# Optimization experiments

Hardware: AMD Instinct MI355X
Metric: run time of the kernel (lower is better)

Reference implementation:

```python
import jax, jax.numpy as jnp
import numpy as np

N_IN, N_OUT, D_IN, D_HID, STYLE = 16384, 16384, 64, 256, 64
E = 1048576
EPS_BN = 1e-5
EPS_ADA = 1e-8
SLOPE = 0.2

def leaky(x):
    return jnp.where(x >= 0, x, SLOPE * x)

def bn_train(h, g, b):
    # BatchNorm1d, training mode: batch stats over dim 0, biased variance
    m = jnp.mean(h, axis=0)
    v = jnp.var(h, axis=0)
    return (h - m) * jax.lax.rsqrt(v + EPS_BN) * g + b

def adain(h, style, w1, b1, w2, b2):
    # per-node instance norm over feature axis (unbiased std, as torch.std),
    # style-conditioned per-feature gamma/beta
    mean = jnp.mean(h, axis=1, keepdims=True)
    std = jnp.std(h, axis=1, ddof=1, keepdims=True)
    gamma = w1 @ style + b1
    beta = w2 @ style + b2
    return gamma * (h - mean) / (std + EPS_ADA) + beta

def gat_conv(h, src, dst, W, att_src, att_dst, bias):
    # PyG GATConv, heads=1: linear -> edge attention -> segment softmax -> scatter
    xs = h @ W.T                          # [N, D_IN]
    a_s = xs @ att_src                    # [N]
    a_d = xs @ att_dst                    # [N]
    e = leaky(a_s[src] + a_d[dst])        # [E]
    emax = jax.ops.segment_max(e, dst, num_segments=N_OUT)
    emax = jnp.where(jnp.isfinite(emax), emax, 0.0)
    ex = jnp.exp(e - emax[dst])
    den = jax.ops.segment_sum(ex, dst, num_segments=N_OUT)
    alpha = ex / den[dst]                 # softmax over incoming edges per dst
    out = jax.ops.segment_sum(alpha[:, None] * xs[src], dst, num_segments=N_OUT)
    return out + bias

def setup_inputs():
    key = jax.random.key(0)
    ks = jax.random.split(key, 24)
    p = lambda k, shape: jax.random.normal(k, shape, jnp.float32) * 0.05
    return {
        "x": jax.random.normal(ks[0], (N_IN, D_IN), jnp.float32),
        "style": jax.random.normal(ks[1], (STYLE,), jnp.float32),
        "edge_index": jax.random.randint(ks[2], (2, E), 0, N_OUT, jnp.int32),
        "trs_w": p(ks[3], (N_OUT, N_IN)), "trs_b": jnp.zeros((N_OUT,), jnp.float32),
        "bn2_g": jnp.ones((N_OUT,), jnp.float32), "bn2_b": jnp.zeros((N_OUT,), jnp.float32),
        "fc1_w": p(ks[4], (D_HID, D_IN)), "fc1_b": jnp.zeros((D_HID,), jnp.float32),
        "bn1_g": jnp.ones((D_HID,), jnp.float32), "bn1_b": jnp.zeros((D_HID,), jnp.float32),
        "gat_w": p(ks[5], (D_IN, D_HID)),
        "gat_att_src": p(ks[6], (D_IN,)), "gat_att_dst": p(ks[7], (D_IN,)),
        "gat_b": jnp.zeros((D_IN,), jnp.float32),
        "a1_w1": p(ks[8], (D_IN, STYLE)), "a1_b1": jnp.zeros((D_IN,), jnp.float32),
        "a1_w2": p(ks[9], (D_IN, STYLE)), "a1_b2": jnp.zeros((D_IN,), jnp.float32),
        "a2_w1": p(ks[10], (D_HID, STYLE)), "a2_b1": jnp.zeros((D_HID,), jnp.float32),
        "a2_w2": p(ks[11], (D_HID, STYLE)), "a2_b2": jnp.zeros((D_HID,), jnp.float32),
        "a3_w1": p(ks[12], (D_IN, STYLE)), "a3_b1": jnp.zeros((D_IN,), jnp.float32),
        "a3_w2": p(ks[13], (D_IN, STYLE)), "a3_b2": jnp.zeros((D_IN,), jnp.float32),
    }

def reference(x, style, edge_index, trs_w, trs_b, bn2_g, bn2_b, fc1_w, fc1_b, bn1_g, bn1_b, gat_w, gat_att_src, gat_att_dst, gat_b, a1_w1, a1_b1, a1_w2, a1_b2, a2_w1, a2_b1, a2_w2, a2_b2, a3_w1, a3_b1, a3_w2, a3_b2):
    h = x.T @ trs_w.T + trs_b                 # [D_IN, N_OUT]
    h = leaky(bn_train(h, bn2_g, bn2_b))      # dropout: eval-mode identity
    h = h.T                                    # [N_OUT, D_IN]
    h = adain(h, style, a1_w1, a1_b1, a1_w2, a1_b2)
    h = leaky(bn_train(h @ fc1_w.T + fc1_b, bn1_g, bn1_b))  # [N_OUT, D_HID]
    h = adain(h, style, a2_w1, a2_b1, a2_w2, a2_b2)
    src, dst = edge_index[0], edge_index[1]
    h = leaky(gat_conv(h, src, dst, gat_w, gat_att_src, gat_att_dst, gat_b))
    h = adain(h, style, a3_w1, a3_b1, a3_w2, a3_b2)
    return h
```

## Files before the change

### kernel.cpp

```cpp
#include <hip/hip_runtime.h>
#include <hip/hip_bf16.h>

#define N_NODES 16384
#define NEDGE   1048576

typedef __attribute__((ext_vector_type(4))) float f32x4;
typedef __attribute__((ext_vector_type(4))) unsigned u32x4;
typedef __attribute__((ext_vector_type(8))) short bf16x8;
typedef unsigned short u16;

__device__ __forceinline__ short f2bf(float f) {
  union { float f; unsigned u; } v; v.f = f;
  unsigned r = v.u + 0x7FFFu + ((v.u >> 16) & 1u);
  return (short)(r >> 16);
}
__device__ __forceinline__ unsigned pk2(float lo, float hi) {
  __hip_bfloat162 h = __float22bfloat162_rn(make_float2(lo, hi));
  return *reinterpret_cast<unsigned*>(&h);
}
__device__ __forceinline__ bf16x8 cvt8(f32x4 a, f32x4 b) {
  u32x4 u;
  u[0] = pk2(a[0], a[1]); u[1] = pk2(a[2], a[3]);
  u[2] = pk2(b[0], b[1]); u[3] = pk2(b[2], b[3]);
  return __builtin_bit_cast(bf16x8, u);
}
__device__ __forceinline__ float red16(float v) {
  v += __shfl_xor(v, 1); v += __shfl_xor(v, 2);
  v += __shfl_xor(v, 4); v += __shfl_xor(v, 8);
  return v;
}
__device__ __forceinline__ float red64(float v) {
  v += __shfl_xor(v, 1); v += __shfl_xor(v, 2); v += __shfl_xor(v, 4);
  v += __shfl_xor(v, 8); v += __shfl_xor(v, 16); v += __shfl_xor(v, 32);
  return v;
}
__device__ __forceinline__ float lrelu(float x){ return x >= 0.f ? x : 0.2f*x; }

__global__ __launch_bounds__(256) void k_prep(
    const float* __restrict__ x, const float* __restrict__ style,
    const float* __restrict__ fc1_w, const float* __restrict__ gat_w,
    const float* __restrict__ a1w1, const float* __restrict__ a1b1,
    const float* __restrict__ a1w2, const float* __restrict__ a1b2,
    const float* __restrict__ a2w1, const float* __restrict__ a2b1,
    const float* __restrict__ a2w2, const float* __restrict__ a2b2,
    const float* __restrict__ a3w1, const float* __restrict__ a3b1,
    const float* __restrict__ a3w2, const float* __restrict__ a3b2,
    u16* __restrict__ xpk, u16* __restrict__ fc1pk, u16* __restrict__ gatpk,
    float* __restrict__ gb, const int* __restrict__ dst, int* __restrict__ cnt)
{
  if (blockIdx.x >= 531) {
    int t = ((blockIdx.x - 531) << 8) + threadIdx.x;
    #pragma unroll
    for (int i = 0; i < 4; ++i) atomicAdd(&cnt[dst[t + i*262144]], 1);
    return;
  }
  int tid = blockIdx.x * 256 + threadIdx.x;
  if (tid < 131072) {
    int lane = tid & 63;
    int kt = tid >> 8, nt = (tid >> 6) & 3;
    int k0 = kt*32 + (lane>>4)*8, c = nt*16 + (lane&15);
    bf16x8 o;
    #pragma unroll
    for (int j = 0; j < 8; ++j) o[j] = f2bf(x[(size_t)(k0+j)*64 + c]);
    ((bf16x8*)xpk)[tid] = o;
  } else if (tid < 133120) {
    int t2 = tid - 131072;
    int lane = t2 & 63, kt = t2 >> 10, nt = (t2 >> 6) & 15;
    int k0 = kt*32 + (lane>>4)*8, c = nt*16 + (lane&15);
    bf16x8 o;
    #pragma unroll
    for (int j = 0; j < 8; ++j) o[j] = f2bf(fc1_w[(size_t)c*64 + k0 + j]);
    ((bf16x8*)fc1pk)[t2] = o;
  } else if (tid < 135168) {
    int t3 = tid - 133120;
    int lane = t3 & 63, kt = t3 >> 8, nt = (t3 >> 6) & 3;
    int k0 = kt*32 + (lane>>4)*8, c = nt*16 + (lane&15);
    bf16x8 o;
    #pragma unroll
    for (int j = 0; j < 8; ++j) o[j] = f2bf(gat_w[(size_t)c*256 + k0 + j]);
    ((bf16x8*)gatpk)[t3] = o;
  } else if (tid < 135936) {
    int t4 = tid - 135168;
    const float* wp; const float* bp; float* op; int d;
    if (t4 < 64)       { wp=a1w1; bp=a1b1; op=gb;       d=t4; }
    else if (t4 < 128) { wp=a1w2; bp=a1b2; op=gb+64;    d=t4-64; }
    else if (t4 < 384) { wp=a2w1; bp=a2b1; op=gb+128;   d=t4-128; }
    else if (t4 < 640) { wp=a2w2; bp=a2b2; op=gb+384;   d=t4-384; }
    else if (t4 < 704) { wp=a3w1; bp=a3b1; op=gb+640;   d=t4-640; }
    else               { wp=a3w2; bp=a3b2; op=gb+704;   d=t4-704; }
    float s = bp[d];
    for (int k = 0; k < 64; ++k) s += wp[(size_t)d*64 + k] * style[k];
    op[d] = s;
  }
}

__global__ __launch_bounds__(256, 4) void k_gemm12(
    const float* __restrict__ W, const u16* __restrict__ xpk,
    const float* __restrict__ trs_b, const float* __restrict__ bn2_g,
    const float* __restrict__ bn2_b, const float* __restrict__ g1,
    const float* __restrict__ be1,
    const u16* __restrict__ fc1pk, const float* __restrict__ fc1_b,
    float* __restrict__ H3, float* __restrict__ colsum, float* __restrict__ colsq)
{
  const int tid  = threadIdx.x;
  const int lane = tid & 63;
  const int wv   = tid >> 6;
  const int jb   = blockIdx.x << 4;
  const int c0   = lane & 15, kg = lane >> 4;
  const int sw   = c0 & 7;

  __shared__ __align__(16) float lbuf[2][4096];
  __shared__ float h2t[16 * 68];

  const float* gsrc[4];
  int ldst[4];
  #pragma unroll
  for (int i = 0; i < 4; ++i) {
    int r = wv + (i << 2);
    gsrc[i] = W + (size_t)(jb + r) * 16384 + (size_t)((lane ^ (r & 7)) << 2);
    ldst[i] = ((r << 6) + lane) << 2;
  }

  const int it0 = blockIdx.x & 63;
  f32x4 z = {0.f,0.f,0.f,0.f};
  f32x4 acc = z;

  {
    int kk = it0 << 8;
    #pragma unroll
    for (int i = 0; i < 4; ++i) {
      f32x4 v = __builtin_nontemporal_load((const f32x4*)(gsrc[i] + kk));
      *(f32x4*)&lbuf[0][ldst[i]] = v;
    }
  }
  __syncthreads();

  const bf16x8* xb = ((const bf16x8*)xpk) + (wv << 6) + lane;

  int buf = 0;
  for (int it = 0; it < 64; ++it) {
    f32x4 vn[4];
    const bool hasNext = (it + 1) < 64;
    if (hasNext) {
      int kk = ((it + 1 + it0) & 63) << 8;
      #pragma unroll
      for (int i = 0; i < 4; ++i)
        vn[i] = __builtin_nontemporal_load((const f32x4*)(gsrc[i] + kk));
    }
    {
      int ktg0 = ((it + it0) & 63) << 3;
      const float* lb = lbuf[buf] + (c0 << 8);
      const bf16x8* bp = xb + (size_t)ktg0 * 256;
      #pragma unroll
      for (int kt = 0; kt < 8; ++kt) {
        int u0 = (kt << 3) + (kg << 1);
        f32x4 a0 = *(const f32x4*)(lb + ((u0 ^ sw) << 2));
        f32x4 a1 = *(const f32x4*)(lb + (((u0 + 1) ^ sw) << 2));
        bf16x8 b = bp[(size_t)kt << 8];
        acc = __builtin_amdgcn_mfma_f32_16x16x32_bf16(cvt8(a0, a1), b, acc, 0,0,0);
      }
    }
    if (hasNext) {
      float* lo = lbuf[buf ^ 1];
      #pragma unroll
      for (int i = 0; i < 4; ++i) *(f32x4*)&lo[ldst[i]] = vn[i];
    }
    __syncthreads();
    buf ^= 1;
  }

  #pragma unroll
  for (int i = 0; i < 4; ++i)
    h2t[((kg << 2) + i) * 68 + (wv << 4) + c0] = acc[i];
  __syncthreads();

  #pragma unroll
  for (int i = 0; i < 4; ++i) {
    int jr = (wv << 2) + i;
    int j  = jb + jr;
    float v = h2t[jr * 68 + lane] + trs_b[j];
    float s = red64(v), q = red64(v * v);
    float mean = s * 0.015625f;
    float var  = q * 0.015625f - mean * mean;
    float inv  = rsqrtf(var + 1e-5f) * bn2_g[j];
    v = lrelu((v - mean) * inv + bn2_b[j]);
    s = red64(v); q = red64(v * v);
    mean = s * 0.015625f;
    var  = q * 0.015625f - mean * mean;
    float sd = sqrtf(fmaxf(var, 0.f) * (64.f / 63.f));
    float id = 1.f / (sd + 1e-8f);
    h2t[jr * 68 + lane] = g1[lane] * (v - mean) * id + be1[lane];
  }
  __syncthreads();

  const float* ha = h2t + c0 * 68 + (kg << 3);
  bf16x8 a0 = cvt8(*(const f32x4*)ha,        *(const f32x4*)(ha+4));
  bf16x8 a1 = cvt8(*(const f32x4*)(ha+32),   *(const f32x4*)(ha+36));
  const bf16x8* fpv = ((const bf16x8*)fc1pk) + lane;
  f32x4 acc2[4] = {z,z,z,z};
  #pragma unroll
  for (int q = 0; q < 4; ++q) {
    int nt = (wv << 2) | q;
    acc2[q] = __builtin_amdgcn_mfma_f32_16x16x32_bf16(a0, fpv[nt*64],      acc2[q], 0,0,0);
    acc2[q] = __builtin_amdgcn_mfma_f32_16x16x32_bf16(a1, fpv[(16+nt)*64], acc2[q], 0,0,0);
  }
  #pragma unroll
  for (int q = 0; q < 4; ++q) {
    int c = (((wv << 2) | q) << 4) + c0;
    float bias = fc1_b[c];
    float cs = 0.f, cq = 0.f;
    #pragma unroll
    for (int r = 0; r < 4; ++r) {
      float v = acc2[q][r] + bias;
      H3[(size_t)(jb + (kg<<2) + r) * 256 + c] = v;
      cs += v; cq += v*v;
    }
    cs += __shfl_xor(cs, 16); cs += __shfl_xor(cs, 32);
    cq += __shfl_xor(cq, 16); cq += __shfl_xor(cq, 32);
    if (kg == 0) { atomicAdd(&colsum[c], cs); atomicAdd(&colsq[c], cq); }
  }
}

__global__ __launch_bounds__(256) void k_gemm3(
    const float* __restrict__ H3, const float* __restrict__ colsum,
    const float* __restrict__ colsq, const float* __restrict__ bn1_g,
    const float* __restrict__ bn1_b, const float* __restrict__ gb,
    const u16* __restrict__ gatpk,
    const float* __restrict__ att_s, const float* __restrict__ att_d,
    float* __restrict__ xs, float* __restrict__ a_s, float* __restrict__ a_d,
    const int* __restrict__ cnt, int* __restrict__ off, int* __restrict__ cur)
{
  if (blockIdx.x == 1024) {
    __shared__ int ps[256];
    int t = threadIdx.x;
    int base = t * 64;
    int s = 0;
    for (int i = 0; i < 64; ++i) s += cnt[base + i];
    ps[t] = s;
    __syncthreads();
    for (int d = 1; d < 256; d <<= 1) {
      int v = (t >= d) ? ps[t - d] : 0;
      __syncthreads();
      ps[t] += v;
      __syncthreads();
    }
    int run = ps[t] - s;
    for (int i = 0; i < 64; ++i) {
      off[base + i] = run; cur[base + i] = run;
      run += cnt[base + i];
    }
    return;
  }
  const int lane = threadIdx.x & 63, wv = threadIdx.x >> 6;
  const int jb = blockIdx.x << 4;
  const int c0 = lane & 15, kg = lane >> 4;
  const int row = jb + c0;
  const int col0 = (wv << 6) + (kg << 3);
  const float* g2  = gb + 128;
  const float* be2 = gb + 384;

  f32x4 w4[4];
  float ps = 0.f, pq = 0.f;
  #pragma unroll
  for (int kk = 0; kk < 2; ++kk) {
    #pragma unroll
    for (int h = 0; h < 2; ++h) {
      int c = col0 + kk*32 + h*4;
      f32x4 v  = *(const f32x4*)(H3 + (size_t)row*256 + c);
      f32x4 cm = *(const f32x4*)(colsum + c);
      f32x4 cq = *(const f32x4*)(colsq + c);
      f32x4 gg = *(const f32x4*)(bn1_g + c);
      f32x4 bb = *(const f32x4*)(bn1_b + c);
      f32x4 t;
      #pragma unroll
      for (int i = 0; i < 4; ++i) {
        float m  = cm[i] * (1.f/16384.f);
        float va = cq[i] * (1.f/16384.f) - m*m;
        float u  = (v[i]-m) * rsqrtf(va + 1e-5f) * gg[i] + bb[i];
        u = lrelu(u);
        t[i] = u; ps += u; pq += u*u;
      }
      w4[kk*2+h] = t;
    }
  }
  ps += __shfl_xor(ps, 16); ps += __shfl_xor(ps, 32);
  pq += __shfl_xor(pq, 16); pq += __shfl_xor(pq, 32);
  __shared__ float sps[64], sqs[64];
  if (kg == 0) { sps[(wv<<4) + c0] = ps; sqs[(wv<<4) + c0] = pq; }
  __syncthreads();
  float rs = sps[c0] + sps[16+c0] + sps[32+c0] + sps[48+c0];
  float rq = sqs[c0] + sqs[16+c0] + sqs[32+c0] + sqs[48+c0];
  float mean = rs * (1.f/256.f);
  float var  = rq * (1.f/256.f) - mean*mean;
  float sd   = sqrtf(fmaxf(var, 0.f) * (256.f/255.f));
  float id   = 1.f / (sd + 1e-8f);
  bf16x8 afr[2];
  #pragma unroll
  for (int kk = 0; kk < 2; ++kk) {
    f32x4 o[2];
    #pragma unroll
    for (int h = 0; h < 2; ++h) {
      int c = col0 + kk*32 + h*4;
      f32x4 ga = *(const f32x4*)(g2 + c);
      f32x4 bd = *(const f32x4*)(be2 + c);
      #pragma unroll
      for (int i = 0; i < 4; ++i) o[h][i] = ga[i]*(w4[kk*2+h][i]-mean)*id + bd[i];
    }
    afr[kk] = cvt8(o[0], o[1]);
  }
  const bf16x8* bpv = ((const bf16x8*)gatpk) + lane;
  f32x4 z = {0.f,0.f,0.f,0.f};
  f32x4 acc[4] = {z,z,z,z};
  #pragma unroll
  for (int kk = 0; kk < 2; ++kk) {
    int kt = (wv << 1) | kk;
    #pragma unroll
    for (int nt = 0; nt < 4; ++nt)
      acc[nt] = __builtin_amdgcn_mfma_f32_16x16x32_bf16(afr[kk], bpv[((kt<<2)+nt)*64], acc[nt], 0,0,0);
  }
  __shared__ float lred[3 * 16 * 64];
  if (wv) {
    float* rp = lred + ((wv - 1) << 10) + lane;
    #pragma unroll
    for (int nt = 0; nt < 4; ++nt)
      #pragma unroll
      for (int r = 0; r < 4; ++r) rp[((nt<<2)+r)<<6] = acc[nt][r];
  }
  __syncthreads();
  if (wv) return;
  float as0 = att_s[c0], as1 = att_s[c0+16], as2 = att_s[c0+32], as3 = att_s[c0+48];
  float ad0 = att_d[c0], ad1 = att_d[c0+16], ad2 = att_d[c0+32], ad3 = att_d[c0+48];
  const float* rp = lred + lane;
  #pragma unroll
  for (int r = 0; r < 4; ++r) {
    int j = jb + (kg << 2) + r;
    float v[4];
    #pragma unroll
    for (int nt = 0; nt < 4; ++nt) {
      int idx = ((nt<<2)+r)<<6;
      v[nt] = acc[nt][r] + rp[idx] + rp[idx+1024] + rp[idx+2048];
    }
    float* op = xs + (size_t)j * 64 + c0;
    op[0] = v[0]; op[16] = v[1]; op[32] = v[2]; op[48] = v[3];
    float ss = red16(v[0]*as0 + v[1]*as1 + v[2]*as2 + v[3]*as3);
    float dd = red16(v[0]*ad0 + v[1]*ad1 + v[2]*ad2 + v[3]*ad3);
    if (c0 == 0) { a_s[j] = ss; a_d[j] = dd; }
  }
}

__global__ __launch_bounds__(256) void k_scatter(
    const int* __restrict__ src, const int* __restrict__ dst,
    int* __restrict__ cur, int* __restrict__ ssrc)
{
  int t = (blockIdx.x << 8) + threadIdx.x;
  #pragma unroll
  for (int i = 0; i < 4; ++i) {
    int e = t + i * 262144;
    int s = src[e], d = dst[e];
    int p = atomicAdd(&cur[d], 1);
    ssrc[p] = s;
  }
}

__global__ __launch_bounds__(256) void k_gat(
    const int* __restrict__ cnt, const int* __restrict__ off,
    const int* __restrict__ ssrc, const float* __restrict__ a_s,
    const float* __restrict__ a_d,
    const float* __restrict__ xs, const float* __restrict__ gat_b,
    const float* __restrict__ g3, const float* __restrict__ be3,
    float* __restrict__ out)
{
  const int lane = threadIdx.x & 63, wv = threadIdx.x >> 6;
  const int j = (blockIdx.x << 2) | wv;
  const int n = cnt[j], beg = off[j];
  const int c4 = (lane & 15) << 2;
  const int eq = lane >> 4;
  const float adj = a_d[j];
  f32x4 acc = {0.f,0.f,0.f,0.f};
  float den = 0.f;
  if (n > 0) {
    for (int ch = 0; ch < n; ch += 64) {
      int k = ch + lane;
      bool ok = k < n;
      int   s = ok ? ssrc[beg + k] : 0;
      float p = ok ? __expf(lrelu(a_s[s] + adj)) : 0.f;
      den += p;
      int m = n - ch; if (m > 64) m = 64;
      int iters = (m + 3) >> 2;
      for (int i = 0; i < iters; ++i) {
        int idx = (i << 2) | eq;
        float pi = __shfl(p, idx);
        int   si = __shfl(s, idx);
        f32x4 v = *(const f32x4*)(xs + (size_t)si * 64 + c4);
        acc += pi * v;
      }
    }
    den = red64(den);
    #pragma unroll
    for (int i = 0; i < 4; ++i) { acc[i] += __shfl_xor(acc[i], 16); acc[i] += __shfl_xor(acc[i], 32); }
    float rd = 1.f / den;
    acc *= rd;
  }
  f32x4 gbv = *(const f32x4*)(gat_b + c4);
  float v0 = lrelu(acc[0] + gbv[0]);
  float v1 = lrelu(acc[1] + gbv[1]);
  float v2 = lrelu(acc[2] + gbv[2]);
  float v3 = lrelu(acc[3] + gbv[3]);
  float s = red16(v0+v1+v2+v3);
  float q = red16(v0*v0+v1*v1+v2*v2+v3*v3);
  float mean = s * (1.f/64.f);
  float var  = q * (1.f/64.f) - mean*mean;
  float sd   = sqrtf(fmaxf(var, 0.f) * (64.f/63.f));
  float id   = 1.f / (sd + 1e-8f);
  if (eq == 0) {
    f32x4 gv = *(const f32x4*)(g3 + c4);
    f32x4 bv = *(const f32x4*)(be3 + c4);
    f32x4 o;
    o[0] = gv[0]*(v0-mean)*id + bv[0];
    o[1] = gv[1]*(v1-mean)*id + bv[1];
    o[2] = gv[2]*(v2-mean)*id + bv[2];
    o[3] = gv[3]*(v3-mean)*id + bv[3];
    *(f32x4*)(out + (size_t)j * 64 + c4) = o;
  }
}

extern "C" void kernel_launch(void* const* d_in, const int* in_sizes, int n_in,
                              void* d_out, int out_size, void* d_ws, size_t ws_size,
                              hipStream_t stream) {
  (void)in_sizes; (void)n_in; (void)out_size; (void)ws_size;
  const float* x      = (const float*)d_in[0];
  const float* style  = (const float*)d_in[1];
  const int*   ei     = (const int*)d_in[2];
  const float* trs_w  = (const float*)d_in[3];
  const float* trs_b  = (const float*)d_in[4];
  const float* bn2_g  = (const float*)d_in[5];
  const float* bn2_b  = (const float*)d_in[6];
  const float* fc1_w  = (const float*)d_in[7];
  const float* fc1_b  = (const float*)d_in[8];
  const float* bn1_g  = (const float*)d_in[9];
  const float* bn1_b  = (const float*)d_in[10];
  const float* gat_w  = (const float*)d_in[11];
  const float* att_s  = (const float*)d_in[12];
  const float* att_d  = (const float*)d_in[13];
  const float* gat_b  = (const float*)d_in[14];
  const float* a1w1   = (const float*)d_in[15];
  const float* a1b1   = (const float*)d_in[16];
  const float* a1w2   = (const float*)d_in[17];
  const float* a1b2   = (const float*)d_in[18];
  const float* a2w1   = (const float*)d_in[19];
  const float* a2b1   = (const float*)d_in[20];
  const float* a2w2   = (const float*)d_in[21];
  const float* a2b2   = (const float*)d_in[22];
  const float* a3w1   = (const float*)d_in[23];
  const float* a3b1   = (const float*)d_in[24];
  const float* a3w2   = (const float*)d_in[25];
  const float* a3b2   = (const float*)d_in[26];

  char* ws = (char*)d_ws;
  u16*   xpk    = (u16*)(ws);
  u16*   fc1pk  = (u16*)(ws + 2097152);
  u16*   gatpk  = (u16*)(ws + 2129920);
  float* gb     = (float*)(ws + 2162688);
  float* H3     = (float*)(ws + 6361088);
  float* xs     = (float*)(ws + 39915520);
  float* as_    = (float*)(ws + 44109824);
  float* ad_    = (float*)(ws + 44175360);
  float* colsum = (float*)(ws + 44240896);
  float* colsq  = (float*)(ws + 44241920);
  int*   cnt    = (int*)(ws + 44242944);
  int*   off    = (int*)(ws + 44308480);
  int*   cur    = (int*)(ws + 44374016);
  int*   ssrc   = (int*)(ws + 44439552);

  hipMemsetAsync(colsum, 0, 2048, stream);
  hipMemsetAsync(cnt, 0, 65536, stream);

  k_prep<<<1555, 256, 0, stream>>>(x, style, fc1_w, gat_w,
      a1w1, a1b1, a1w2, a1b2, a2w1, a2b1, a2w2, a2b2, a3w1, a3b1, a3w2, a3b2,
      xpk, fc1pk, gatpk, gb, ei + NEDGE, cnt);
  k_gemm12<<<1024, 256, 0, stream>>>(trs_w, xpk, trs_b, bn2_g, bn2_b,
      gb, gb + 64, fc1pk, fc1_b, H3, colsum, colsq);
  k_gemm3<<<1025, 256, 0, stream>>>(H3, colsum, colsq, bn1_g, bn1_b, gb,
      gatpk, att_s, att_d, xs, as_, ad_, cnt, off, cur);
  k_scatter<<<1024, 256, 0, stream>>>(ei, ei + NEDGE, cur, ssrc);
  k_gat<<<4096, 256, 0, stream>>>(cnt, off, ssrc, as_, ad_, xs, gat_b,
      gb + 640, gb + 704, (float*)d_out);
}
```

Baseline: 397.3 us.

## Use direct global-to-LDS 4-stage pipeline in GEMM and fold scan/scatter into GEMM kernels

Replaces the register-staged double buffer in the big trs_w GEMM with global_load_lds direct-to-LDS loads over four smaller stages, issued three iterations ahead and gated by explicit vmcnt waits and barriers. This is meant to hide HBM latency better and cut the VGPR round trip. The CSR prefix scan moves into an extra block of k_gemm12, and the edge scatter moves into extra blocks of k_gemm3, removing one kernel launch and letting that work overlap the GEMMs. The hand-written waitcnt counts and the reliance on extra-block scheduling order are easy to get subtly wrong.

```diff
diff --git a/kernel.cpp b/kernel.cpp
--- a/kernel.cpp
+++ b/kernel.cpp
@@ -100,8 +100,30 @@
     const float* __restrict__ bn2_b, const float* __restrict__ g1,
     const float* __restrict__ be1,
     const u16* __restrict__ fc1pk, const float* __restrict__ fc1_b,
-    float* __restrict__ H3, float* __restrict__ colsum, float* __restrict__ colsq)
+    float* __restrict__ H3, float* __restrict__ colsum, float* __restrict__ colsq,
+    const int* __restrict__ cnt, int* __restrict__ off, int* __restrict__ cur)
 {
+  if (blockIdx.x == 1024) {
+    __shared__ int ps[256];
+    int t = threadIdx.x;
+    int base = t * 64;
+    int s = 0;
+    for (int i = 0; i < 64; ++i) s += cnt[base + i];
+    ps[t] = s;
+    __syncthreads();
+    for (int d = 1; d < 256; d <<= 1) {
+      int v = (t >= d) ? ps[t - d] : 0;
+      __syncthreads();
+      ps[t] += v;
+      __syncthreads();
+    }
+    int run = ps[t] - s;
+    for (int i = 0; i < 64; ++i) {
+      off[base + i] = run; cur[base + i] = run;
+      run += cnt[base + i];
+    }
+    return;
+  }
   const int tid  = threadIdx.x;
   const int lane = tid & 63;
   const int wv   = tid >> 6;
@@ -109,65 +131,64 @@
   const int c0   = lane & 15, kg = lane >> 4;
   const int sw   = c0 & 7;
 
-  __shared__ __align__(16) float lbuf[2][4096];
+  __shared__ __align__(16) float lbuf[4][2048];
   __shared__ float h2t[16 * 68];
 
-  const float* gsrc[4];
-  int ldst[4];
-  #pragma unroll
-  for (int i = 0; i < 4; ++i) {
-    int r = wv + (i << 2);
-    gsrc[i] = W + (size_t)(jb + r) * 16384 + (size_t)((lane ^ (r & 7)) << 2);
-    ldst[i] = ((r << 6) + lane) << 2;
-  }
-
-  const int it0 = blockIdx.x & 63;
+  const int r0 = (wv << 2) | (lane >> 5);
+  const int r1 = r0 + 2;
+  const float* gA = W + (size_t)(jb + r0) * 16384 + (((lane & 31) ^ (r0 & 7)) << 2);
+  const float* gB = W + (size_t)(jb + r1) * 16384 + (((lane & 31) ^ (r1 & 7)) << 2);
+
+  const int it0 = blockIdx.x & 127;
   f32x4 z = {0.f,0.f,0.f,0.f};
   f32x4 acc = z;
-
-  {
-    int kk = it0 << 8;
-    #pragma unroll
-    for (int i = 0; i < 4; ++i) {
-      f32x4 v = __builtin_nontemporal_load((const f32x4*)(gsrc[i] + kk));
-      *(f32x4*)&lbuf[0][ldst[i]] = v;
-    }
-  }
+  const bf16x8* xb = ((const bf16x8*)xpk) + (wv << 6) + lane;
+
+#define ISSUE(itx) do { \
+    int b_ = (itx) & 3; \
+    size_t go_ = (size_t)((((itx) + it0) & 127) << 7); \
+    __builtin_amdgcn_global_load_lds( \
+        (const __attribute__((address_space(1))) void*)(gA + go_), \
+        (__attribute__((address_space(3))) void*)&lbuf[b_][wv << 9], 16, 0, 0); \
+    __builtin_amdgcn_global_load_lds( \
+        (const __attribute__((address_space(1))) void*)(gB + go_), \
+        (__attribute__((address_space(3))) void*)&lbuf[b_][(wv << 9) + 256], 16, 0, 0); \
+  } while (0)
+
+#define COMPUTE(itx) do { \
+    int b_ = (itx) & 3; \
+    int ktg0_ = (((itx) + it0) & 127) << 2; \
+    const float* lb_ = &lbuf[b_][c0 << 7]; \
+    const bf16x8* bp_ = xb + (size_t)ktg0_ * 256; \
+    _Pragma("unroll") \
+    for (int kt = 0; kt < 4; ++kt) { \
+      int u0_ = (kt << 3) + (kg << 1); \
+      f32x4 a0 = *(const f32x4*)(lb_ + ((u0_ ^ sw) << 2)); \
+      f32x4 a1 = *(const f32x4*)(lb_ + (((u0_ + 1) ^ sw) << 2)); \
+      bf16x8 b = bp_[(size_t)kt << 8]; \
+      acc = __builtin_amdgcn_mfma_f32_16x16x32_bf16(cvt8(a0, a1), b, acc, 0,0,0); \
+    } \
+  } while (0)
+
+  ISSUE(0); ISSUE(1); ISSUE(2);
+  for (int it = 0; it < 126; ++it) {
+    asm volatile("s_waitcnt vmcnt(4)" ::: "memory");
+    __builtin_amdgcn_sched_barrier(0);
+    __builtin_amdgcn_s_barrier();
+    if (it < 125) ISSUE(it + 3);
+    COMPUTE(it);
+  }
+  asm volatile("s_waitcnt vmcnt(2)" ::: "memory");
+  __builtin_amdgcn_sched_barrier(0);
+  __builtin_amdgcn_s_barrier();
+  COMPUTE(126);
+  asm volatile("s_waitcnt vmcnt(0)" ::: "memory");
+  __builtin_amdgcn_sched_barrier(0);
+  __builtin_amdgcn_s_barrier();
+  COMPUTE(127);
+#undef ISSUE
+#undef COMPUTE
   __syncthreads();
-
-  const bf16x8* xb = ((const bf16x8*)xpk) + (wv << 6) + lane;
-
-  int buf = 0;
-  for (int it = 0; it < 64; ++it) {
-    f32x4 vn[4];
-    const bool hasNext = (it + 1) < 64;
-    if (hasNext) {
-      int kk = ((it + 1 + it0) & 63) << 8;
-      #pragma unroll
-      for (int i = 0; i < 4; ++i)
-        vn[i] = __builtin_nontemporal_load((const f32x4*)(gsrc[i] + kk));
-    }
-    {
-      int ktg0 = ((it + it0) & 63) << 3;
-      const float* lb = lbuf[buf] + (c0 << 8);
-      const bf16x8* bp = xb + (size_t)ktg0 * 256;
-      #pragma unroll
-      for (int kt = 0; kt < 8; ++kt) {
-        int u0 = (kt << 3) + (kg << 1);
-        f32x4 a0 = *(const f32x4*)(lb + ((u0 ^ sw) << 2));
-        f32x4 a1 = *(const f32x4*)(lb + (((u0 + 1) ^ sw) << 2));
-        bf16x8 b = bp[(size_t)kt << 8];
-        acc = __builtin_amdgcn_mfma_f32_16x16x32_bf16(cvt8(a0, a1), b, acc, 0,0,0);
-      }
-    }
-    if (hasNext) {
-      float* lo = lbuf[buf ^ 1];
-      #pragma unroll
-      for (int i = 0; i < 4; ++i) *(f32x4*)&lo[ldst[i]] = vn[i];
-    }
-    __syncthreads();
-    buf ^= 1;
-  }
 
   #pragma unroll
   for (int i = 0; i < 4; ++i)
@@ -228,26 +249,17 @@
     const u16* __restrict__ gatpk,
     const float* __restrict__ att_s, const float* __restrict__ att_d,
     float* __restrict__ xs, float* __restrict__ a_s, float* __restrict__ a_d,
-    const int* __restrict__ cnt, int* __restrict__ off, int* __restrict__ cur)
+    const int* __restrict__ src, const int* __restrict__ dstE,
+    int* __restrict__ cur, int* __restrict__ ssrc)
 {
-  if (blockIdx.x == 1024) {
-    __shared__ int ps[256];
-    int t = threadIdx.x;
-    int base = t * 64;
-    int s = 0;
-    for (int i = 0; i < 64; ++i) s += cnt[base + i];
-    ps[t] = s;
-    __syncthreads();
-    for (int d = 1; d < 256; d <<= 1) {
-      int v = (t >= d) ? ps[t - d] : 0;
-      __syncthreads();
-      ps[t] += v;
-      __syncthreads();
-    }
-    int run = ps[t] - s;
-    for (int i = 0; i < 64; ++i) {
-      off[base + i] = run; cur[base + i] = run;
-      run += cnt[base + i];
+  if (blockIdx.x >= 1024) {
+    int t = ((blockIdx.x - 1024) << 8) + threadIdx.x;
+    #pragma unroll
+    for (int i = 0; i < 4; ++i) {
+      int e = t + i * 262144;
+      int s = src[e], d = dstE[e];
+      int p = atomicAdd(&cur[d], 1);
+      ssrc[p] = s;
     }
     return;
   }
@@ -345,20 +357,6 @@
     float ss = red16(v[0]*as0 + v[1]*as1 + v[2]*as2 + v[3]*as3);
     float dd = red16(v[0]*ad0 + v[1]*ad1 + v[2]*ad2 + v[3]*ad3);
     if (c0 == 0) { a_s[j] = ss; a_d[j] = dd; }
-  }
-}
-
-__global__ __launch_bounds__(256) void k_scatter(
-    const int* __restrict__ src, const int* __restrict__ dst,
-    int* __restrict__ cur, int* __restrict__ ssrc)
-{
-  int t = (blockIdx.x << 8) + threadIdx.x;
-  #pragma unroll
-  for (int i = 0; i < 4; ++i) {
-    int e = t + i * 262144;
-    int s = src[e], d = dst[e];
-    int p = atomicAdd(&cur[d], 1);
-    ssrc[p] = s;
   }
 }
 
@@ -478,11 +476,10 @@
   k_prep<<<1555, 256, 0, stream>>>(x, style, fc1_w, gat_w,
       a1w1, a1b1, a1w2, a1b2, a2w1, a2b1, a2w2, a2b2, a3w1, a3b1, a3w2, a3b2,
       xpk, fc1pk, gatpk, gb, ei + NEDGE, cnt);
-  k_gemm12<<<1024, 256, 0, stream>>>(trs_w, xpk, trs_b, bn2_g, bn2_b,
-      gb, gb + 64, fc1pk, fc1_b, H3, colsum, colsq);
-  k_gemm3<<<1025, 256, 0, stream>>>(H3, colsum, colsq, bn1_g, bn1_b, gb,
-      gatpk, att_s, att_d, xs, as_, ad_, cnt, off, cur);
-  k_scatter<<<1024, 256, 0, stream>>>(ei, ei + NEDGE, cur, ssrc);
+  k_gemm12<<<1025, 256, 0, stream>>>(trs_w, xpk, trs_b, bn2_g, bn2_b,
+      gb, gb + 64, fc1pk, fc1_b, H3, colsum, colsq, cnt, off, cur);
+  k_gemm3<<<2048, 256, 0, stream>>>(H3, colsum, colsq, bn1_g, bn1_b, gb,
+      gatpk, att_s, att_d, xs, as_, ad_, ei, ei + NEDGE, cur, ssrc);
   k_gat<<<4096, 256, 0, stream>>>(cnt, off, ssrc, as_, ad_, xs, gat_b,
       gb + 640, gb + 704, (float*)d_out);
 }
```

After: 432.7 us (median of 4 runs). 1.09x slower.
